# Performance work log

Measured on AMD Instinct MI355X. Metric: run time of the kernel, lower is better.

Reference implementation:

```python
import jax, jax.numpy as jnp
import numpy as np

N = 100000
E = 1600000
IN_DIM, HID, HEADS, OUT_DIM = 128, 64, 4, 40
NEG_SLOPE = 0.2
BN_EPS = 1e-5


def gat_conv(x, src, dst, W, att_src, att_dst, bias, heads, out_c, concat):
    # x: [N, F_in]; src/dst: [E'] (self-loops included)
    h = (x @ W).reshape(-1, heads, out_c)                      # [N, H, C]
    a_src = jnp.sum(h * att_src[None], axis=-1)                # [N, H]
    a_dst = jnp.sum(h * att_dst[None], axis=-1)                # [N, H]
    e = jax.nn.leaky_relu(a_src[src] + a_dst[dst], NEG_SLOPE)  # [E', H]
    # segment softmax over destination neighborhoods
    m = jax.ops.segment_max(e, dst, num_segments=N)            # [N, H]
    e = jnp.exp(e - m[dst])
    s = jax.ops.segment_sum(e, dst, num_segments=N)            # [N, H]
    alpha = e / (s[dst] + 1e-16)                               # [E', H]
    msg = h[src] * alpha[:, :, None]                           # [E', H, C]
    out = jax.ops.segment_sum(msg, dst, num_segments=N)        # [N, H, C]
    out = out.reshape(N, heads * out_c) if concat else out.mean(axis=1)
    return out + bias


def batch_norm(x, g, b, m, v):
    return (x - m) * (g / jnp.sqrt(v + BN_EPS)) + b


def setup_inputs() -> dict:
    key = jax.random.key(0)
    ks = jax.random.split(key, 16)
    rn = lambda k, shp, s=0.1: jax.random.normal(k, shp, jnp.float32) * s
    inp = {}
    inp['x'] = jax.random.normal(ks[0], (N, IN_DIM), jnp.float32)
    inp['edge_index'] = jax.random.randint(ks[1], (2, E), 0, N, jnp.int64)
    inp['W1'] = rn(ks[2], (IN_DIM, HEADS * HID))
    inp['att_src1'] = rn(ks[3], (HEADS, HID))
    inp['att_dst1'] = rn(ks[4], (HEADS, HID))
    inp['b1'] = rn(ks[5], (HEADS * HID,))
    inp['bn1_g'] = jax.random.uniform(ks[6], (HEADS * HID,), jnp.float32)
    inp['bn1_b'] = rn(ks[7], (HEADS * HID,))
    inp['bn1_m'] = jnp.zeros((HEADS * HID,), jnp.float32)
    inp['bn1_v'] = jnp.ones((HEADS * HID,), jnp.float32)
    inp['W2'] = rn(ks[8], (HEADS * HID, HID))
    inp['att_src2'] = rn(ks[9], (1, HID))
    inp['att_dst2'] = rn(ks[10], (1, HID))
    inp['b2'] = rn(ks[11], (HID,))
    inp['bn2_g'] = jax.random.uniform(ks[12], (HID,), jnp.float32)
    inp['bn2_b'] = rn(ks[13], (HID,))
    inp['bn2_m'] = jnp.zeros((HID,), jnp.float32)
    inp['bn2_v'] = jnp.ones((HID,), jnp.float32)
    inp['W3'] = rn(ks[14], (HID, OUT_DIM))
    k3 = jax.random.split(ks[15], 3)
    inp['att_src3'] = rn(k3[0], (1, OUT_DIM))
    inp['att_dst3'] = rn(k3[1], (1, OUT_DIM))
    inp['b3'] = rn(k3[2], (OUT_DIM,))
    return inp


def reference(x, edge_index, W1, att_src1, att_dst1, b1, bn1_g, bn1_b, bn1_m, bn1_v,
              W2, att_src2, att_dst2, b2, bn2_g, bn2_b, bn2_m, bn2_v,
              W3, att_src3, att_dst3, b3):
    # add self-loops (PyG GATConv default)
    loop = jnp.arange(N, dtype=edge_index.dtype)
    src = jnp.concatenate([edge_index[0], loop])
    dst = jnp.concatenate([edge_index[1], loop])
    # eval mode: dropout = identity, BN uses running stats
    h = gat_conv(x, src, dst, W1, att_src1, att_dst1, b1, HEADS, HID, True)
    h = jax.nn.elu(batch_norm(h, bn1_g, bn1_b, bn1_m, bn1_v))
    h = gat_conv(h, src, dst, W2, att_src2, att_dst2, b2, 1, HID, False)
    h = jax.nn.elu(batch_norm(h, bn2_g, bn2_b, bn2_m, bn2_v))
    out = gat_conv(h, src, dst, W3, att_src3, att_dst3, b3, 1, OUT_DIM, False)
    return jax.nn.log_softmax(out, axis=1)
```

## Files before the change

kernel.cpp:

```cpp
#include <hip/hip_runtime.h>
#include <hip/hip_fp16.h>
#include <cstdint>

#define IN_DIM   128
#define HIDC     64
#define HEADS    4
#define OUT_DIM  40
#define NEG_SLOPE 0.2f
#define BN_EPS   1e-5f

typedef unsigned short ushortt;
typedef float fx4 __attribute__((ext_vector_type(4)));
typedef short bf16x8 __attribute__((ext_vector_type(8)));

__device__ __forceinline__ float bfval(ushortt u) {
    return __uint_as_float(((unsigned)u) << 16);
}
__device__ __forceinline__ ushortt f2bf(float f) {
    unsigned u = __float_as_uint(f);
    u += 0x7fffu + ((u >> 16) & 1u);
    return (ushortt)(u >> 16);
}
__device__ __forceinline__ unsigned pack2bf(float a, float b) {
    return (unsigned)f2bf(a) | ((unsigned)f2bf(b) << 16);
}

__device__ __forceinline__ void acc8(float* acc, float a, uint4 h) {
    unsigned u;
    u = h.x;
    acc[0] = fmaf(a, __uint_as_float(u << 16), acc[0]);
    acc[1] = fmaf(a, __uint_as_float(u & 0xffff0000u), acc[1]);
    u = h.y;
    acc[2] = fmaf(a, __uint_as_float(u << 16), acc[2]);
    acc[3] = fmaf(a, __uint_as_float(u & 0xffff0000u), acc[3]);
    u = h.z;
    acc[4] = fmaf(a, __uint_as_float(u << 16), acc[4]);
    acc[5] = fmaf(a, __uint_as_float(u & 0xffff0000u), acc[5]);
    u = h.w;
    acc[6] = fmaf(a, __uint_as_float(u << 16), acc[6]);
    acc[7] = fmaf(a, __uint_as_float(u & 0xffff0000u), acc[7]);
}

__global__ void detect_kernel(const unsigned int* __restrict__ e, int* __restrict__ flag) {
    __shared__ int any;
    if (threadIdx.x == 0) any = 0;
    __syncthreads();
    for (int i = threadIdx.x; i < 1024; i += 256)
        if (e[2 * i + 1] != 0u) any = 1;
    __syncthreads();
    if (threadIdx.x == 0) flag[0] = any ? 0 : 1;
}

__device__ __forceinline__ int load_idx(const int* ei, int is64, long long pos) {
    return is64 ? ei[2 * pos] : ei[pos];
}

__global__ void hist_kernel(const int* __restrict__ ei, const int* __restrict__ flag,
                            int* __restrict__ deg, int E, int Etot) {
    int i = blockIdx.x * 256 + threadIdx.x;
    if (i >= Etot) return;
    int is64 = flag[0];
    int dst = (i < E) ? load_idx(ei, is64, (long long)E + i) : (i - E);
    atomicAdd(&deg[dst], 1);
}

__global__ void scan_kernel(int* __restrict__ data, int n) {
    __shared__ int wsum[16];
    __shared__ int chunk_total;
    int lane = threadIdx.x & 63;
    int w = threadIdx.x >> 6;
    int carry = 0;
    for (int base = 0; base < n; base += 1024) {
        int i = base + (int)threadIdx.x;
        int v = (i < n) ? data[i] : 0;
        int x = v;
        #pragma unroll
        for (int ofs = 1; ofs < 64; ofs <<= 1) {
            int y = __shfl_up(x, ofs);
            if (lane >= ofs) x += y;
        }
        if (lane == 63) wsum[w] = x;
        __syncthreads();
        if (w == 0) {
            int s = (lane < 16) ? wsum[lane] : 0;
            #pragma unroll
            for (int ofs = 1; ofs < 16; ofs <<= 1) {
                int y = __shfl_up(s, ofs);
                if (lane >= ofs) s += y;
            }
            if (lane < 16) wsum[lane] = s;
            if (lane == 15) chunk_total = s;
        }
        __syncthreads();
        int woff = (w > 0) ? wsum[w - 1] : 0;
        if (i < n) data[i] = (x + woff) - v + carry;
        int ct = chunk_total;
        __syncthreads();
        carry += ct;
    }
}

__global__ void scatter_kernel(const int* __restrict__ ei, const int* __restrict__ flag,
                               int* __restrict__ cursor, int* __restrict__ csr,
                               int* __restrict__ dstv, int E, int Etot) {
    int i = blockIdx.x * 256 + threadIdx.x;
    if (i >= Etot) return;
    int is64 = flag[0];
    int src, dst;
    if (i < E) {
        src = load_idx(ei, is64, i);
        dst = load_idx(ei, is64, (long long)E + i);
    } else {
        src = dst = i - E;
    }
    int pos = atomicAdd(&cursor[dst], 1);
    csr[pos] = src;
    dstv[pos] = dst;
}

__global__ void prep_bn_kernel(const float* b1, const float* g1, const float* bb1,
                               const float* m1, const float* v1,
                               const float* b2, const float* g2, const float* bb2,
                               const float* m2, const float* v2,
                               float* __restrict__ bnsc, float* __restrict__ bnsh) {
    int t = threadIdx.x;
    if (t < 256) {
        float s = g1[t] * rsqrtf(v1[t] + BN_EPS);
        bnsc[t] = s;
        bnsh[t] = (b1[t] - m1[t]) * s + bb1[t];
    } else if (t < 320) {
        int c = t - 256;
        float s = g2[c] * rsqrtf(v2[c] + BN_EPS);
        bnsc[t] = s;
        bnsh[t] = (b2[c] - m2[c]) * s + bb2[c];
    }
}

__global__ void castx_kernel(const float* __restrict__ x, ushortt* __restrict__ xb, int n8) {
    int i = blockIdx.x * 256 + threadIdx.x;
    if (i >= n8) return;
    const float4* src = (const float4*)(x + (size_t)i * 8);
    float4 v0 = src[0], v1 = src[1];
    uint4 pk = make_uint4(pack2bf(v0.x, v0.y), pack2bf(v0.z, v0.w),
                          pack2bf(v1.x, v1.y), pack2bf(v1.z, v1.w));
    *(uint4*)(xb + (size_t)i * 8) = pk;
}

__global__ void prep_wt_kernel(const float* __restrict__ W, ushortt* __restrict__ WT,
                               int K, int Norig, int Npad) {
    int i = blockIdx.x * 256 + threadIdx.x;
    if (i >= K * Npad) return;
    int n = i / K, k = i % K;
    WT[i] = (n < Norig) ? f2bf(W[(size_t)k * Norig + n]) : (ushortt)0;
}

template <int K, int NCATT, bool L1MODE>
__launch_bounds__(256)
__global__ void gemm_mfma_kernel(const ushortt* __restrict__ A, const ushortt* __restrict__ BT,
                                 ushortt* __restrict__ hB,
                                 const float* __restrict__ atts, const float* __restrict__ attd,
                                 float* __restrict__ a_s, float* __restrict__ a_d, int M) {
    __shared__ ushortt Abuf[64][40];
    __shared__ ushortt Bbuf[64][40];
    int m0 = blockIdx.x * 64;
    int head = L1MODE ? blockIdx.y : 0;
    int n0g = head * 64;
    int t = threadIdx.x;
    int w = t >> 6, l = t & 63;
    int colg = l & 15, kg = l >> 4;
    int srow = t >> 2, sseg = t & 3;

    fx4 acc[4] = {};

    for (int k0 = 0; k0 < K; k0 += 32) {
        uint4 av = make_uint4(0u, 0u, 0u, 0u);
        if (m0 + srow < M)
            av = *(const uint4*)(A + (size_t)(m0 + srow) * K + k0 + sseg * 8);
        *(uint4*)&Abuf[srow][sseg * 8] = av;
        uint4 bv = *(const uint4*)(BT + (size_t)(n0g + srow) * K + k0 + sseg * 8);
        *(uint4*)&Bbuf[srow][sseg * 8] = bv;
        __syncthreads();
        bf16x8 a = *(const bf16x8*)&Abuf[w * 16 + colg][kg * 8];
        #pragma unroll
        for (int bt = 0; bt < 4; ++bt) {
            bf16x8 b = *(const bf16x8*)&Bbuf[bt * 16 + colg][kg * 8];
            acc[bt] = __builtin_amdgcn_mfma_f32_16x16x32_bf16(a, b, acc[bt], 0, 0, 0);
        }
        __syncthreads();
    }

    const int nstride = L1MODE ? 256 : 64;
    float ps[4] = {}, pd[4] = {};
    #pragma unroll
    for (int bt = 0; bt < 4; ++bt) {
        int cl = bt * 16 + colg;
        float as_v = (cl < NCATT) ? atts[n0g + cl] : 0.f;
        float ad_v = (cl < NCATT) ? attd[n0g + cl] : 0.f;
        #pragma unroll
        for (int i = 0; i < 4; ++i) {
            int m = m0 + w * 16 + kg * 4 + i;
            if (m < M)
                hB[(size_t)m * nstride + n0g + cl] = f2bf(acc[bt][i]);
            ps[i] = fmaf(acc[bt][i], as_v, ps[i]);
            pd[i] = fmaf(acc[bt][i], ad_v, pd[i]);
        }
    }
    #pragma unroll
    for (int o = 1; o < 16; o <<= 1) {
        #pragma unroll
        for (int i = 0; i < 4; ++i) {
            ps[i] += __shfl_xor(ps[i], o);
            pd[i] += __shfl_xor(pd[i], o);
        }
    }
    if (colg == 0) {
        #pragma unroll
        for (int i = 0; i < 4; ++i) {
            int m = m0 + w * 16 + kg * 4 + i;
            if (m < M) {
                if constexpr (L1MODE) {
                    a_s[(size_t)m * 4 + head] = ps[i];
                    a_d[(size_t)m * 4 + head] = pd[i];
                } else {
                    a_s[m] = ps[i];
                    a_d[m] = pd[i];
                }
            }
        }
    }
}

__launch_bounds__(256)
__global__ void alpha4e_kernel(const int* __restrict__ csr, const int* __restrict__ dstv,
                               const float* __restrict__ a_s4, const float* __restrict__ a_d4,
                               __half* __restrict__ alH, int Etot) {
    int j = blockIdx.x * 256 + threadIdx.x;
    if (j >= Etot) return;
    int s = csr[j], d = dstv[j];
    fx4 as = *(const fx4*)&a_s4[(size_t)s * 4];
    fx4 ad = *(const fx4*)&a_d4[(size_t)d * 4];
    #pragma unroll
    for (int h = 0; h < 4; ++h) {
        float v = as[h] + ad[h];
        v = v > 0.f ? v : NEG_SLOPE * v;
        alH[(size_t)h * Etot + j] = __float2half(__expf(v));
    }
}

__launch_bounds__(256)
__global__ void alpha1e_kernel(const int* __restrict__ csr, const int* __restrict__ dstv,
                               const float* __restrict__ a_s, const float* __restrict__ a_d,
                               __half* __restrict__ alE, int Etot) {
    int j = blockIdx.x * 256 + threadIdx.x;
    if (j >= Etot) return;
    float v = a_s[csr[j]] + a_d[dstv[j]];
    v = v > 0.f ? v : NEG_SLOPE * v;
    alE[j] = __float2half(__expf(v));
}

__launch_bounds__(256)
__global__ void pv1_kernel(const int* __restrict__ off, const int* __restrict__ csr,
                           const __half* __restrict__ alH, const ushortt* __restrict__ hB,
                           const float* __restrict__ bnsc, const float* __restrict__ bnsh,
                           ushortt* __restrict__ actb, int N, int Etot) {
    int node = blockIdx.x * 4 + (threadIdx.x >> 6);
    int lane = threadIdx.x & 63;
    if (node >= N) return;
    int half = lane >> 5, sub = lane & 31, head = sub >> 3;
    unsigned subb = (unsigned)(sub * 16);
    int beg = off[node], end = off[node + 1], deg = end - beg;
    const __half* alh = alH + (size_t)head * Etot;
    const char* hBb = (const char*)hB;
    float acc[8] = {};
    float ssum = 0.f;
    int nt = (deg + 1) >> 1;
    int j = beg + half;
    int t = 0;
    for (; t + 4 <= nt; t += 4, j += 8) {
        float av[4]; unsigned ro[4];
        #pragma unroll
        for (int q = 0; q < 4; ++q) {
            int jq = j + 2 * q;
            bool v = jq < end;
            int idx = v ? jq : beg;
            int s = csr[idx];
            av[q] = v ? __half2float(alh[idx]) : 0.f;
            ro[q] = (unsigned)s * 512u + subb;
        }
        uint4 h0 = *(const uint4*)(hBb + ro[0]);
        uint4 h1 = *(const uint4*)(hBb + ro[1]);
        uint4 h2 = *(const uint4*)(hBb + ro[2]);
        uint4 h3 = *(const uint4*)(hBb + ro[3]);
        acc8(acc, av[0], h0);
        acc8(acc, av[1], h1);
        acc8(acc, av[2], h2);
        acc8(acc, av[3], h3);
        ssum += (av[0] + av[1]) + (av[2] + av[3]);
    }
    for (; t < nt; ++t, j += 2) {
        bool v = j < end;
        int idx = v ? j : beg;
        int s = csr[idx];
        float a = v ? __half2float(alh[idx]) : 0.f;
        uint4 h = *(const uint4*)(hBb + (unsigned)s * 512u + subb);
        acc8(acc, a, h);
        ssum += a;
    }
    #pragma unroll
    for (int i = 0; i < 8; ++i) acc[i] += __shfl_xor(acc[i], 32);
    ssum += __shfl_xor(ssum, 32);
    if (half == 0) {
        float inv = 1.f / (ssum + 1e-16f);
        int g = sub * 8;
        float o[8];
        #pragma unroll
        for (int i = 0; i < 8; ++i) {
            float v = acc[i] * inv * bnsc[g + i] + bnsh[g + i];
            o[i] = v > 0.f ? v : expm1f(v);
        }
        uint4 pk = make_uint4(pack2bf(o[0], o[1]), pack2bf(o[2], o[3]),
                              pack2bf(o[4], o[5]), pack2bf(o[6], o[7]));
        *(uint4*)&actb[(size_t)node * 256 + g] = pk;
    }
}

__launch_bounds__(256)
__global__ void pv2_kernel(const int* __restrict__ off, const int* __restrict__ csr,
                           const __half* __restrict__ alE, const ushortt* __restrict__ hB,
                           const float* __restrict__ bnsc, const float* __restrict__ bnsh,
                           ushortt* __restrict__ act2b, int N) {
    int node = blockIdx.x * 4 + (threadIdx.x >> 6);
    int lane = threadIdx.x & 63;
    if (node >= N) return;
    int grp = lane >> 3, sub = lane & 7;
    unsigned subb = (unsigned)(sub * 16);
    int beg = off[node], end = off[node + 1], deg = end - beg;
    const char* hBb = (const char*)hB;
    float acc[8] = {};
    float ssum = 0.f;
    int nt = (deg + 7) >> 3;
    int j = beg + grp;
    int t = 0;
    for (; t + 2 <= nt; t += 2, j += 16) {
        int jA = j, jB = j + 8;
        bool vA = jA < end, vB = jB < end;
        int iA = vA ? jA : beg, iB = vB ? jB : beg;
        int sA = csr[iA], sB = csr[iB];
        float aA = vA ? __half2float(alE[iA]) : 0.f;
        float aB = vB ? __half2float(alE[iB]) : 0.f;
        uint4 hA = *(const uint4*)(hBb + (unsigned)sA * 128u + subb);
        uint4 hBv = *(const uint4*)(hBb + (unsigned)sB * 128u + subb);
        acc8(acc, aA, hA);
        acc8(acc, aB, hBv);
        ssum += aA + aB;
    }
    for (; t < nt; ++t, j += 8) {
        bool v = j < end;
        int idx = v ? j : beg;
        int s = csr[idx];
        float a = v ? __half2float(alE[idx]) : 0.f;
        uint4 h = *(const uint4*)(hBb + (unsigned)s * 128u + subb);
        acc8(acc, a, h);
        ssum += a;
    }
    #pragma unroll
    for (int o = 8; o <= 32; o <<= 1) {
        #pragma unroll
        for (int i = 0; i < 8; ++i) acc[i] += __shfl_xor(acc[i], o);
        ssum += __shfl_xor(ssum, o);
    }
    if (lane < 8) {
        float inv = 1.f / (ssum + 1e-16f);
        int g = lane * 8;
        float o[8];
        #pragma unroll
        for (int i = 0; i < 8; ++i) {
            float v = acc[i] * inv * bnsc[256 + g + i] + bnsh[256 + g + i];
            o[i] = v > 0.f ? v : expm1f(v);
        }
        uint4 pk = make_uint4(pack2bf(o[0], o[1]), pack2bf(o[2], o[3]),
                              pack2bf(o[4], o[5]), pack2bf(o[6], o[7]));
        *(uint4*)&act2b[(size_t)node * 64 + g] = pk;
    }
}

__launch_bounds__(256)
__global__ void pv3_kernel(const int* __restrict__ off, const int* __restrict__ csr,
                           const __half* __restrict__ alE, const ushortt* __restrict__ hB,
                           const float* __restrict__ bias, float* __restrict__ out, int N) {
    int node = blockIdx.x * 4 + (threadIdx.x >> 6);
    int lane = threadIdx.x & 63;
    if (node >= N) return;
    int grp = lane >> 3, sub = lane & 7;
    unsigned subb = (unsigned)(sub * 16);
    int beg = off[node], end = off[node + 1];
    const char* hBb = (const char*)hB;
    float acc[8] = {};
    float ssum = 0.f;
    for (int j0 = beg; j0 < end; j0 += 8) {
        int j = j0 + grp;
        bool v = j < end;
        int idx = v ? j : beg;
        int s = csr[idx];
        float a = v ? __half2float(alE[idx]) : 0.f;
        uint4 h = *(const uint4*)(hBb + (unsigned)s * 128u + subb);
        acc8(acc, a, h);
        ssum += a;
    }
    #pragma unroll
    for (int o = 8; o <= 32; o <<= 1) {
        #pragma unroll
        for (int i = 0; i < 8; ++i) acc[i] += __shfl_xor(acc[i], o);
        ssum += __shfl_xor(ssum, o);
    }
    float inv = 1.f / (ssum + 1e-16f);
    int g = lane * 8;
    bool act8 = lane < 5;
    float val[8];
    float mx = -INFINITY;
    #pragma unroll
    for (int i = 0; i < 8; ++i) {
        val[i] = act8 ? (acc[i] * inv + bias[act8 ? (g + i) : 0]) : -INFINITY;
        mx = fmaxf(mx, val[i]);
    }
    #pragma unroll
    for (int o = 1; o < 8; o <<= 1) mx = fmaxf(mx, __shfl_xor(mx, o));
    float se = 0.f;
    if (act8) {
        #pragma unroll
        for (int i = 0; i < 8; ++i) se += __expf(val[i] - mx);
    }
    #pragma unroll
    for (int o = 1; o < 8; o <<= 1) se += __shfl_xor(se, o);
    if (act8) {
        float lse = mx + logf(se);
        float* dst = &out[(size_t)node * 40 + g];
        fx4 v0 = {val[0] - lse, val[1] - lse, val[2] - lse, val[3] - lse};
        fx4 v1 = {val[4] - lse, val[5] - lse, val[6] - lse, val[7] - lse};
        *(fx4*)dst = v0;
        *(fx4*)(dst + 4) = v1;
    }
}

extern "C" void kernel_launch(void* const* d_in, const int* in_sizes, int n_in,
                              void* d_out, int out_size, void* d_ws, size_t ws_size,
                              hipStream_t stream) {
    const float* x      = (const float*)d_in[0];
    const int*   ei     = (const int*)d_in[1];
    const float* W1     = (const float*)d_in[2];
    const float* att_s1 = (const float*)d_in[3];
    const float* att_d1 = (const float*)d_in[4];
    const float* b1     = (const float*)d_in[5];
    const float* bn1g   = (const float*)d_in[6];
    const float* bn1b   = (const float*)d_in[7];
    const float* bn1m   = (const float*)d_in[8];
    const float* bn1v   = (const float*)d_in[9];
    const float* W2     = (const float*)d_in[10];
    const float* att_s2 = (const float*)d_in[11];
    const float* att_d2 = (const float*)d_in[12];
    const float* b2     = (const float*)d_in[13];
    const float* bn2g   = (const float*)d_in[14];
    const float* bn2b   = (const float*)d_in[15];
    const float* bn2m   = (const float*)d_in[16];
    const float* bn2v   = (const float*)d_in[17];
    const float* W3     = (const float*)d_in[18];
    const float* att_s3 = (const float*)d_in[19];
    const float* att_d3 = (const float*)d_in[20];
    const float* b3     = (const float*)d_in[21];

    const int N    = in_sizes[0] / IN_DIM;
    const int E    = in_sizes[1] / 2;
    const int Etot = E + N;

    int*   wsi = (int*)d_ws;
    float* wsf = (float*)d_ws;
    size_t p = 0;
    int*   off    = wsi + p; p += (size_t)N + 16;  p = (p + 3) & ~(size_t)3;
    int*   cursor = wsi + p; p += (size_t)N;       p = (p + 3) & ~(size_t)3;
    int*   flag   = wsi + p; p += 16;
    int*   csr    = wsi + p; p += (size_t)Etot;    p = (p + 3) & ~(size_t)3;
    int*   dstv   = wsi + p; p += (size_t)Etot;    p = (p + 3) & ~(size_t)3;
    float* a_s4   = wsf + p; p += (size_t)N * 4;
    float* a_d4   = wsf + p; p += (size_t)N * 4;
    float* bnsc   = wsf + p; p += 384;
    float* bnsh   = wsf + p; p += 384;
    ushortt* xb   = (ushortt*)(wsf + p); p += (size_t)N * 64;
    ushortt* W1T  = (ushortt*)(wsf + p); p += (256 * 128) / 2 + 16;
    ushortt* W2T  = (ushortt*)(wsf + p); p += (64 * 256) / 2 + 16;
    ushortt* W3T  = (ushortt*)(wsf + p); p += (64 * 64) / 2 + 16;
    size_t H = p;            p += (size_t)N * 128;
    size_t A1 = p;           p += (size_t)N * 128;
    size_t A2 = p;           p += (size_t)N * 32;
    __half* alH = (__half*)(wsf + p); p += (size_t)Etot * 2 + 16;
    if (ws_size < p * 4) return;

    ushortt* hB1   = (ushortt*)(wsf + H);
    ushortt* hB23  = (ushortt*)(wsf + H);
    ushortt* actb  = (ushortt*)(wsf + A1);
    ushortt* act2b = (ushortt*)(wsf + A2);
    __half*  alE   = alH;

    float* outp = (float*)d_out;

    hipMemsetAsync(off, 0, ((size_t)N + 1) * sizeof(int), stream);
    detect_kernel<<<1, 256, 0, stream>>>((const unsigned int*)ei, flag);
    {
        int blocks = (Etot + 255) / 256;
        hist_kernel<<<blocks, 256, 0, stream>>>(ei, flag, off, E, Etot);
        scan_kernel<<<1, 1024, 0, stream>>>(off, N + 1);
        hipMemcpyAsync(cursor, off, (size_t)N * sizeof(int), hipMemcpyDeviceToDevice, stream);
        scatter_kernel<<<blocks, 256, 0, stream>>>(ei, flag, cursor, csr, dstv, E, Etot);
    }
    prep_bn_kernel<<<1, 384, 0, stream>>>(b1, bn1g, bn1b, bn1m, bn1v,
                                          b2, bn2g, bn2b, bn2m, bn2v, bnsc, bnsh);
    prep_wt_kernel<<<(256 * 128 + 255) / 256, 256, 0, stream>>>(W1, W1T, 128, 256, 256);
    prep_wt_kernel<<<(64 * 256 + 255) / 256, 256, 0, stream>>>(W2, W2T, 256, 64, 64);
    prep_wt_kernel<<<(64 * 64 + 255) / 256, 256, 0, stream>>>(W3, W3T, 64, 40, 64);
    castx_kernel<<<((N * 16) + 255) / 256, 256, 0, stream>>>(x, xb, N * 16);

    const int gm64 = (N + 63) / 64;
    const int nb4 = (N + 3) / 4;
    const int eb = (Etot + 255) / 256;

    gemm_mfma_kernel<128, 64, true>
        <<<dim3(gm64, 4), 256, 0, stream>>>(xb, W1T, hB1, att_s1, att_d1, a_s4, a_d4, N);
    alpha4e_kernel<<<eb, 256, 0, stream>>>(csr, dstv, a_s4, a_d4, alH, Etot);
    pv1_kernel<<<nb4, 256, 0, stream>>>(off, csr, alH, hB1, bnsc, bnsh, actb, N, Etot);

    gemm_mfma_kernel<256, 64, false>
        <<<dim3(gm64, 1), 256, 0, stream>>>(actb, W2T, hB23, att_s2, att_d2, a_s4, a_d4, N);
    alpha1e_kernel<<<eb, 256, 0, stream>>>(csr, dstv, a_s4, a_d4, alE, Etot);
    pv2_kernel<<<nb4, 256, 0, stream>>>(off, csr, alE, hB23, bnsc, bnsh, act2b, N);

    gemm_mfma_kernel<64, 40, false>
        <<<dim3(gm64, 1), 256, 0, stream>>>(act2b, W3T, hB23, att_s3, att_d3, a_s4, a_d4, N);
    alpha1e_kernel<<<eb, 256, 0, stream>>>(csr, dstv, a_s4, a_d4, alE, Etot);
    pv3_kernel<<<nb4, 256, 0, stream>>>(off, csr, alE, hB23, b3, outp, N);
}
```

Baseline: 704.4 us.

## Fuse x cast into layer-1 GEMM, merge prep kernels, drop cursor memcpy

The layer-1 GEMM now reads fp32 x directly, converts to bf16 while staging into shared memory, and computes all four heads in one block with the full 256-column weight tile. This removes the separate castx pass and the 4x re-read of A across head blocks. The BN and weight-transpose prep kernels are merged into one launch, and the scan writes the cursor copy itself instead of a device memcpy. The trade-off is a larger accumulator array (16 MFMA tiles) and more shared memory per block, which may lower occupancy.

```diff
diff --git a/kernel.cpp b/kernel.cpp
--- a/kernel.cpp
+++ b/kernel.cpp
@@ -64,7 +64,7 @@
     atomicAdd(&deg[dst], 1);
 }
 
-__global__ void scan_kernel(int* __restrict__ data, int n) {
+__global__ void scan_kernel(int* __restrict__ data, int* __restrict__ cursor, int n) {
     __shared__ int wsum[16];
     __shared__ int chunk_total;
     int lane = threadIdx.x & 63;
@@ -93,7 +93,11 @@
         }
         __syncthreads();
         int woff = (w > 0) ? wsum[w - 1] : 0;
-        if (i < n) data[i] = (x + woff) - v + carry;
+        if (i < n) {
+            int excl = (x + woff) - v + carry;
+            data[i] = excl;
+            if (i < n - 1) cursor[i] = excl;
+        }
         int ct = chunk_total;
         __syncthreads();
         carry += ct;
@@ -118,43 +122,124 @@
     dstv[pos] = dst;
 }
 
-__global__ void prep_bn_kernel(const float* b1, const float* g1, const float* bb1,
-                               const float* m1, const float* v1,
-                               const float* b2, const float* g2, const float* bb2,
-                               const float* m2, const float* v2,
-                               float* __restrict__ bnsc, float* __restrict__ bnsh) {
+__global__ void prep_all_kernel(const float* b1, const float* g1, const float* bb1,
+                                const float* m1, const float* v1,
+                                const float* b2, const float* g2, const float* bb2,
+                                const float* m2, const float* v2,
+                                const float* W1, const float* W2, const float* W3,
+                                float* __restrict__ bnsc, float* __restrict__ bnsh,
+                                ushortt* __restrict__ W1T, ushortt* __restrict__ W2T,
+                                ushortt* __restrict__ W3T) {
+    int i = blockIdx.x * 256 + threadIdx.x;
+    if (i < 320) {
+        if (i < 256) {
+            float s = g1[i] * rsqrtf(v1[i] + BN_EPS);
+            bnsc[i] = s;
+            bnsh[i] = (b1[i] - m1[i]) * s + bb1[i];
+        } else {
+            int c = i - 256;
+            float s = g2[c] * rsqrtf(v2[c] + BN_EPS);
+            bnsc[i] = s;
+            bnsh[i] = (b2[c] - m2[c]) * s + bb2[c];
+        }
+        return;
+    }
+    int j = i - 320;
+    if (j < 256 * 128) {
+        int n = j >> 7, k = j & 127;
+        W1T[j] = f2bf(W1[(size_t)k * 256 + n]);
+        return;
+    }
+    j -= 256 * 128;
+    if (j < 64 * 256) {
+        int n = j >> 8, k = j & 255;
+        W2T[j] = f2bf(W2[(size_t)k * 64 + n]);
+        return;
+    }
+    j -= 64 * 256;
+    if (j < 64 * 64) {
+        int n = j >> 6, k = j & 63;
+        W3T[j] = (n < OUT_DIM) ? f2bf(W3[(size_t)k * OUT_DIM + n]) : (ushortt)0;
+    }
+}
+
+__launch_bounds__(256)
+__global__ void gemm1_mfma_kernel(const float* __restrict__ x, const ushortt* __restrict__ BT,
+                                  ushortt* __restrict__ hB,
+                                  const float* __restrict__ atts, const float* __restrict__ attd,
+                                  float* __restrict__ a_s4, float* __restrict__ a_d4, int M) {
+    __shared__ ushortt Abuf[64][40];
+    __shared__ ushortt Bbuf[256][40];
+    int m0 = blockIdx.x * 64;
     int t = threadIdx.x;
-    if (t < 256) {
-        float s = g1[t] * rsqrtf(v1[t] + BN_EPS);
-        bnsc[t] = s;
-        bnsh[t] = (b1[t] - m1[t]) * s + bb1[t];
-    } else if (t < 320) {
-        int c = t - 256;
-        float s = g2[c] * rsqrtf(v2[c] + BN_EPS);
-        bnsc[t] = s;
-        bnsh[t] = (b2[c] - m2[c]) * s + bb2[c];
-    }
-}
-
-__global__ void castx_kernel(const float* __restrict__ x, ushortt* __restrict__ xb, int n8) {
-    int i = blockIdx.x * 256 + threadIdx.x;
-    if (i >= n8) return;
-    const float4* src = (const float4*)(x + (size_t)i * 8);
-    float4 v0 = src[0], v1 = src[1];
-    uint4 pk = make_uint4(pack2bf(v0.x, v0.y), pack2bf(v0.z, v0.w),
-                          pack2bf(v1.x, v1.y), pack2bf(v1.z, v1.w));
-    *(uint4*)(xb + (size_t)i * 8) = pk;
-}
-
-__global__ void prep_wt_kernel(const float* __restrict__ W, ushortt* __restrict__ WT,
-                               int K, int Norig, int Npad) {
-    int i = blockIdx.x * 256 + threadIdx.x;
-    if (i >= K * Npad) return;
-    int n = i / K, k = i % K;
-    WT[i] = (n < Norig) ? f2bf(W[(size_t)k * Norig + n]) : (ushortt)0;
-}
-
-template <int K, int NCATT, bool L1MODE>
+    int w = t >> 6, l = t & 63;
+    int colg = l & 15, kg = l >> 4;
+    int srow = t >> 2, sseg = t & 3;
+
+    fx4 acc[16] = {};
+
+    for (int k0 = 0; k0 < 128; k0 += 32) {
+        float4 v0 = make_float4(0.f, 0.f, 0.f, 0.f), v1 = v0;
+        if (m0 + srow < M) {
+            const float4* sp = (const float4*)(x + (size_t)(m0 + srow) * 128 + k0 + sseg * 8);
+            v0 = sp[0]; v1 = sp[1];
+        }
+        *(uint4*)&Abuf[srow][sseg * 8] = make_uint4(pack2bf(v0.x, v0.y), pack2bf(v0.z, v0.w),
+                                                    pack2bf(v1.x, v1.y), pack2bf(v1.z, v1.w));
+        #pragma unroll
+        for (int seg = 0; seg < 4; ++seg)
+            *(uint4*)&Bbuf[t][seg * 8] = *(const uint4*)(BT + (size_t)t * 128 + k0 + seg * 8);
+        __syncthreads();
+        bf16x8 a = *(const bf16x8*)&Abuf[w * 16 + colg][kg * 8];
+        #pragma unroll
+        for (int ct = 0; ct < 16; ++ct) {
+            bf16x8 b = *(const bf16x8*)&Bbuf[ct * 16 + colg][kg * 8];
+            acc[ct] = __builtin_amdgcn_mfma_f32_16x16x32_bf16(a, b, acc[ct], 0, 0, 0);
+        }
+        __syncthreads();
+    }
+
+    float ps[4][4] = {}, pd[4][4] = {};
+    #pragma unroll
+    for (int ct = 0; ct < 16; ++ct) {
+        int cl = ct * 16 + colg;
+        int h = cl >> 6;
+        float as_v = atts[cl], ad_v = attd[cl];
+        #pragma unroll
+        for (int i = 0; i < 4; ++i) {
+            int m = m0 + w * 16 + kg * 4 + i;
+            if (m < M)
+                hB[(size_t)m * 256 + cl] = f2bf(acc[ct][i]);
+            ps[i][h] = fmaf(acc[ct][i], as_v, ps[i][h]);
+            pd[i][h] = fmaf(acc[ct][i], ad_v, pd[i][h]);
+        }
+    }
+    #pragma unroll
+    for (int o = 1; o < 16; o <<= 1) {
+        #pragma unroll
+        for (int i = 0; i < 4; ++i)
+            #pragma unroll
+            for (int h = 0; h < 4; ++h) {
+                ps[i][h] += __shfl_xor(ps[i][h], o);
+                pd[i][h] += __shfl_xor(pd[i][h], o);
+            }
+    }
+    if (colg == 0) {
+        #pragma unroll
+        for (int i = 0; i < 4; ++i) {
+            int m = m0 + w * 16 + kg * 4 + i;
+            if (m < M) {
+                #pragma unroll
+                for (int h = 0; h < 4; ++h) {
+                    a_s4[(size_t)m * 4 + h] = ps[i][h];
+                    a_d4[(size_t)m * 4 + h] = pd[i][h];
+                }
+            }
+        }
+    }
+}
+
+template <int K, int NCATT>
 __launch_bounds__(256)
 __global__ void gemm_mfma_kernel(const ushortt* __restrict__ A, const ushortt* __restrict__ BT,
                                  ushortt* __restrict__ hB,
@@ -163,8 +248,6 @@
     __shared__ ushortt Abuf[64][40];
     __shared__ ushortt Bbuf[64][40];
     int m0 = blockIdx.x * 64;
-    int head = L1MODE ? blockIdx.y : 0;
-    int n0g = head * 64;
     int t = threadIdx.x;
     int w = t >> 6, l = t & 63;
     int colg = l & 15, kg = l >> 4;
@@ -177,7 +260,7 @@
         if (m0 + srow < M)
             av = *(const uint4*)(A + (size_t)(m0 + srow) * K + k0 + sseg * 8);
         *(uint4*)&Abuf[srow][sseg * 8] = av;
-        uint4 bv = *(const uint4*)(BT + (size_t)(n0g + srow) * K + k0 + sseg * 8);
+        uint4 bv = *(const uint4*)(BT + (size_t)srow * K + k0 + sseg * 8);
         *(uint4*)&Bbuf[srow][sseg * 8] = bv;
         __syncthreads();
         bf16x8 a = *(const bf16x8*)&Abuf[w * 16 + colg][kg * 8];
@@ -189,18 +272,17 @@
         __syncthreads();
     }
 
-    const int nstride = L1MODE ? 256 : 64;
     float ps[4] = {}, pd[4] = {};
     #pragma unroll
     for (int bt = 0; bt < 4; ++bt) {
         int cl = bt * 16 + colg;
-        float as_v = (cl < NCATT) ? atts[n0g + cl] : 0.f;
-        float ad_v = (cl < NCATT) ? attd[n0g + cl] : 0.f;
+        float as_v = (cl < NCATT) ? atts[cl] : 0.f;
+        float ad_v = (cl < NCATT) ? attd[cl] : 0.f;
         #pragma unroll
         for (int i = 0; i < 4; ++i) {
             int m = m0 + w * 16 + kg * 4 + i;
             if (m < M)
-                hB[(size_t)m * nstride + n0g + cl] = f2bf(acc[bt][i]);
+                hB[(size_t)m * 64 + cl] = f2bf(acc[bt][i]);
             ps[i] = fmaf(acc[bt][i], as_v, ps[i]);
             pd[i] = fmaf(acc[bt][i], ad_v, pd[i]);
         }
@@ -217,15 +299,7 @@
         #pragma unroll
         for (int i = 0; i < 4; ++i) {
             int m = m0 + w * 16 + kg * 4 + i;
-            if (m < M) {
-                if constexpr (L1MODE) {
-                    a_s[(size_t)m * 4 + head] = ps[i];
-                    a_d[(size_t)m * 4 + head] = pd[i];
-                } else {
-                    a_s[m] = ps[i];
-                    a_d[m] = pd[i];
-                }
-            }
+            if (m < M) { a_s[m] = ps[i]; a_d[m] = pd[i]; }
         }
     }
 }
@@ -484,14 +558,13 @@
     float* a_d4   = wsf + p; p += (size_t)N * 4;
     float* bnsc   = wsf + p; p += 384;
     float* bnsh   = wsf + p; p += 384;
-    ushortt* xb   = (ushortt*)(wsf + p); p += (size_t)N * 64;
-    ushortt* W1T  = (ushortt*)(wsf + p); p += (256 * 128) / 2 + 16;
-    ushortt* W2T  = (ushortt*)(wsf + p); p += (64 * 256) / 2 + 16;
-    ushortt* W3T  = (ushortt*)(wsf + p); p += (64 * 64) / 2 + 16;
     size_t H = p;            p += (size_t)N * 128;
     size_t A1 = p;           p += (size_t)N * 128;
     size_t A2 = p;           p += (size_t)N * 32;
     __half* alH = (__half*)(wsf + p); p += (size_t)Etot * 2 + 16;
+    ushortt* W1T = (ushortt*)(wsf + p); p += (256 * 128) / 2 + 16;
+    ushortt* W2T = (ushortt*)(wsf + p); p += (64 * 256) / 2 + 16;
+    ushortt* W3T = (ushortt*)(wsf + p); p += (64 * 64) / 2 + 16;
     if (ws_size < p * 4) return;
 
     ushortt* hB1   = (ushortt*)(wsf + H);
@@ -507,33 +580,31 @@
     {
         int blocks = (Etot + 255) / 256;
         hist_kernel<<<blocks, 256, 0, stream>>>(ei, flag, off, E, Etot);
-        scan_kernel<<<1, 1024, 0, stream>>>(off, N + 1);
-        hipMemcpyAsync(cursor, off, (size_t)N * sizeof(int), hipMemcpyDeviceToDevice, stream);
+        scan_kernel<<<1, 1024, 0, stream>>>(off, cursor, N + 1);
         scatter_kernel<<<blocks, 256, 0, stream>>>(ei, flag, cursor, csr, dstv, E, Etot);
     }
-    prep_bn_kernel<<<1, 384, 0, stream>>>(b1, bn1g, bn1b, bn1m, bn1v,
-                                          b2, bn2g, bn2b, bn2m, bn2v, bnsc, bnsh);
-    prep_wt_kernel<<<(256 * 128 + 255) / 256, 256, 0, stream>>>(W1, W1T, 128, 256, 256);
-    prep_wt_kernel<<<(64 * 256 + 255) / 256, 256, 0, stream>>>(W2, W2T, 256, 64, 64);
-    prep_wt_kernel<<<(64 * 64 + 255) / 256, 256, 0, stream>>>(W3, W3T, 64, 40, 64);
-    castx_kernel<<<((N * 16) + 255) / 256, 256, 0, stream>>>(x, xb, N * 16);
+    {
+        int total = 320 + 256 * 128 + 64 * 256 + 64 * 64;
+        prep_all_kernel<<<(total + 255) / 256, 256, 0, stream>>>(
+            b1, bn1g, bn1b, bn1m, bn1v, b2, bn2g, bn2b, bn2m, bn2v,
+            W1, W2, W3, bnsc, bnsh, W1T, W2T, W3T);
+    }
 
     const int gm64 = (N + 63) / 64;
     const int nb4 = (N + 3) / 4;
     const int eb = (Etot + 255) / 256;
 
-    gemm_mfma_kernel<128, 64, true>
-        <<<dim3(gm64, 4), 256, 0, stream>>>(xb, W1T, hB1, att_s1, att_d1, a_s4, a_d4, N);
+    gemm1_mfma_kernel<<<gm64, 256, 0, stream>>>(x, W1T, hB1, att_s1, att_d1, a_s4, a_d4, N);
     alpha4e_kernel<<<eb, 256, 0, stream>>>(csr, dstv, a_s4, a_d4, alH, Etot);
     pv1_kernel<<<nb4, 256, 0, stream>>>(off, csr, alH, hB1, bnsc, bnsh, actb, N, Etot);
 
-    gemm_mfma_kernel<256, 64, false>
-        <<<dim3(gm64, 1), 256, 0, stream>>>(actb, W2T, hB23, att_s2, att_d2, a_s4, a_d4, N);
+    gemm_mfma_kernel<256, 64><<<gm64, 256, 0, stream>>>(actb, W2T, hB23, att_s2, att_d2,
+                                                        a_s4, a_d4, N);
     alpha1e_kernel<<<eb, 256, 0, stream>>>(csr, dstv, a_s4, a_d4, alE, Etot);
     pv2_kernel<<<nb4, 256, 0, stream>>>(off, csr, alE, hB23, bnsc, bnsh, act2b, N);
 
-    gemm_mfma_kernel<64, 40, false>
-        <<<dim3(gm64, 1), 256, 0, stream>>>(act2b, W3T, hB23, att_s3, att_d3, a_s4, a_d4, N);
+    gemm_mfma_kernel<64, 40><<<gm64, 256, 0, stream>>>(act2b, W3T, hB23, att_s3, att_d3,
+                                                       a_s4, a_d4, N);
     alpha1e_kernel<<<eb, 256, 0, stream>>>(csr, dstv, a_s4, a_d4, alE, Etot);
     pv3_kernel<<<nb4, 256, 0, stream>>>(off, csr, alE, hB23, b3, outp, N);
 }
```

Result: no change. 692.3 us (-1.7%).
